# Performance work log

Measured on AMD Instinct MI355X. Metric: run time of the kernel, lower is better.

The kernel has to match this reference:

```python
import jax, jax.numpy as jnp
import numpy as np

B, D_IN, R, D_P, K, D_C, ITERS = 4096, 2048, 7, 128, 25, 16, 3


def _ln(x, g, b, eps=1e-5):
    m = jnp.mean(x, axis=-1, keepdims=True)
    v = jnp.var(x, axis=-1, keepdims=True)
    return (x - m) * jax.lax.rsqrt(v + eps) * g + b


def _squash(x):
    eps = 1e-6
    ns = jnp.sum(x * x, axis=-1, keepdims=True)
    scale = ns / jnp.maximum(1.0 + ns, eps)
    return scale * x / (jnp.sqrt(ns) + eps)


def setup_inputs() -> dict:
    key = jax.random.key(0)
    ks = jax.random.split(key, 8)
    f = lambda k, shp, s=0.02: (jax.random.normal(k, shp) * s).astype(jnp.float32)
    return {
        "z": jax.random.normal(ks[0], (B, D_IN), jnp.float32),
        "W_prim": f(ks[1], (D_IN, R * D_P)),
        "b_prim": jnp.zeros((R * D_P,), jnp.float32),
        "ln_a_g": jnp.ones((D_IN,), jnp.float32),
        "ln_a_b": jnp.zeros((D_IN,), jnp.float32),
        "W_act": f(ks[2], (D_IN, R)),
        "b_act": jnp.zeros((R,), jnp.float32),
        "w_caps": (np.sqrt(K / (D_P * R)).astype(np.float32)
                   * jax.random.normal(ks[3], (R, D_P, K, D_C))).astype(jnp.float32),
        "ln_c_g": jnp.ones((D_C,), jnp.float32),
        "ln_c_b": jnp.zeros((D_C,), jnp.float32),
        "beta_u": f(ks[4], (K,), 1.0),
        "ln_h_g": jnp.ones((R * D_C,), jnp.float32),
        "ln_h_b": jnp.zeros((R * D_C,), jnp.float32),
        "W_h1": f(ks[5], (R * D_C, 4 * R * D_C)),
        "b_h1": jnp.zeros((4 * R * D_C,), jnp.float32),
        "W_h2": f(ks[6], (4 * R * D_C, 1)),
        "b_h2": jnp.zeros((1,), jnp.float32),
    }


def reference(z, W_prim, b_prim, ln_a_g, ln_a_b, W_act, b_act, w_caps,
              ln_c_g, ln_c_b, beta_u, ln_h_g, ln_h_b, W_h1, b_h1, W_h2, b_h2):
    # primary capsules: [B, R, D_P] poses + [B, R] activations
    pose = _squash((z @ W_prim + b_prim).reshape(B, R, D_P))
    act = jnp.clip(jax.nn.sigmoid(_ln(z, ln_a_g, ln_a_b) @ W_act + b_act), 0.0, 1.0)

    # votes: [B, R, K, D_C]
    u = jnp.einsum('brd,rdkh->brkh', pose, w_caps)
    scale = 1.0 / np.sqrt(D_C).astype(np.float32)

    # iterative routing (EM/softmax-agreement style)
    q = jnp.full((B, R, K), 1.0 / K, dtype=z.dtype)
    class_pose = None
    for _ in range(ITERS):
        wts = q * act[:, :, None]                               # [B,R,K]
        class_pose = _ln(jnp.einsum('brk,brkh->bkh', wts, u), ln_c_g, ln_c_b)
        agree = jnp.einsum('bkh,brkh->brk', class_pose, u) * scale
        q = jax.nn.softmax(agree, axis=-1)

    class_act = jax.nn.sigmoid(beta_u[None, :] + jnp.einsum('brk,br->bk', q, act))
    route_class_emb = q[..., None] * u                          # [B,R,K,D_C]

    # concat per-route interaction vectors -> [B, K, R*D_C]
    class_embed = jnp.transpose(route_class_emb, (0, 2, 1, 3)).reshape(B, K, R * D_C)
    h = jax.nn.gelu(_ln(class_embed, ln_h_g, ln_h_b) @ W_h1 + b_h1, approximate=False)
    logits = (h @ W_h2 + b_h2)[..., 0]                          # [B, K]

    return (logits, class_embed, class_pose, class_act, q, pose, act, route_class_emb)
```

## Files before the change

kernel.cpp:

```cpp
#include <hip/hip_runtime.h>
#include <cstddef>

#define BB 4096
#define DIN 2048
#define RR 7
#define DP 128
#define KK 25
#define DC 16
#define NITERS 3
#define RKH (RR*KK*DC)
#define RK  (RR*KK)
#define KH  (KK*DC)
#define HD  (RR*DC)
#define H4  (4*HD)
#define HEAD_TILES (BB*KK/128)

typedef __attribute__((ext_vector_type(8))) short bf16x8;
typedef __attribute__((ext_vector_type(4))) float f32x4;

__device__ __forceinline__ unsigned pk_bf16(float a, float b) {
    union { float f; unsigned u; } xa, xb;
    xa.f = a; xb.f = b;
    unsigned ua = (xa.u + 0x7FFFu + ((xa.u >> 16) & 1u)) >> 16;
    unsigned ub = (xb.u + 0x7FFFu + ((xb.u >> 16) & 1u)) >> 16;
    return (ua & 0xFFFFu) | (ub << 16);
}

__device__ __forceinline__ float gelu_fast(float x) {
    float u = x * __builtin_fmaf(x * x, 0.07135655f, 1.5957691f);
    u = fmaxf(u, -30.0f);
    float e = __expf(-u);
    return x * __builtin_amdgcn_rcpf(1.0f + e);
}

__global__ __launch_bounds__(256) void transpose_cvt_kernel(
    const float* __restrict__ src, unsigned short* __restrict__ dst, int RS, int CS)
{
    __shared__ float T[64][65];
    int r0 = blockIdx.x * 64, c0 = blockIdx.y * 64;
    size_t bo = (size_t)blockIdx.z * RS * CS;
    src += bo; dst += bo;
    int t = threadIdx.x;
    for (int s = t; s < 64 * 16; s += 256) {
        int row = s >> 4, c4 = s & 15;
        int gr = r0 + row, gc = c0 + c4 * 4;
        float4 v = make_float4(0.f, 0.f, 0.f, 0.f);
        if (gr < RS && gc < CS) v = *(const float4*)(src + (size_t)gr * CS + gc);
        T[row][c4 * 4 + 0] = v.x; T[row][c4 * 4 + 1] = v.y;
        T[row][c4 * 4 + 2] = v.z; T[row][c4 * 4 + 3] = v.w;
    }
    __syncthreads();
    for (int s = t; s < 64 * 16; s += 256) {
        int col = s >> 4, r4 = s & 15;
        int gc = c0 + col, gr = r0 + r4 * 4;
        if (gc < CS && gr + 3 < RS) {
            unsigned lo = pk_bf16(T[r4 * 4 + 0][col], T[r4 * 4 + 1][col]);
            unsigned hi = pk_bf16(T[r4 * 4 + 2][col], T[r4 * 4 + 3][col]);
            *(uint2*)(dst + (size_t)gc * RS + gr) = make_uint2(lo, hi);
        }
    }
}

__global__ __launch_bounds__(256) void w1_frag_kernel(
    const float* __restrict__ W1, unsigned short* __restrict__ W1F)
{
    int d = blockIdx.x * 256 + threadIdx.x;
    int e2 = d & 3;
    int lane = (d >> 2) & 63;
    int fid = d >> 8;
    int j = fid & 3, ks = (fid >> 2) & 3, nc = fid >> 4;
    int col = nc * 64 + j * 16 + (lane & 15);
    int k = ks * 32 + (lane >> 4) * 8 + e2 * 2;
    float a = (k < HD)     ? W1[(size_t)k * H4 + col]       : 0.f;
    float b = (k + 1 < HD) ? W1[(size_t)(k + 1) * H4 + col] : 0.f;
    ((unsigned*)W1F)[d] = pk_bf16(a, b);
}

__global__ __launch_bounds__(256) void wpf_kernel(
    const float* __restrict__ Wp, unsigned short* __restrict__ wpf)
{
    int tid = blockIdx.x * 256 + threadIdx.x;
    int lane = tid & 63;
    int CH = tid >> 6;
    int c = CH & 63, gcol = CH >> 6;
    int n = gcol * 16 + (lane & 15);
    int k0 = c * 32 + (lane >> 4) * 8;
    unsigned d0, d1, d2, d3;
    {
        float a0 = Wp[(size_t)(k0 + 0) * (RR * DP) + n];
        float a1 = Wp[(size_t)(k0 + 1) * (RR * DP) + n];
        float a2 = Wp[(size_t)(k0 + 2) * (RR * DP) + n];
        float a3 = Wp[(size_t)(k0 + 3) * (RR * DP) + n];
        float a4 = Wp[(size_t)(k0 + 4) * (RR * DP) + n];
        float a5 = Wp[(size_t)(k0 + 5) * (RR * DP) + n];
        float a6 = Wp[(size_t)(k0 + 6) * (RR * DP) + n];
        float a7 = Wp[(size_t)(k0 + 7) * (RR * DP) + n];
        d0 = pk_bf16(a0, a1); d1 = pk_bf16(a2, a3);
        d2 = pk_bf16(a4, a5); d3 = pk_bf16(a6, a7);
    }
    *(uint4*)(wpf + (size_t)tid * 8) = make_uint4(d0, d1, d2, d3);
}

__global__ __launch_bounds__(256) void act_kernel(
    const float* __restrict__ z, const float* __restrict__ g, const float* __restrict__ bb,
    const float* __restrict__ Wa, const float* __restrict__ ba,
    float* __restrict__ act_out, unsigned short* __restrict__ zf_out)
{
    int b = blockIdx.x;
    int t = threadIdx.x;
    __shared__ float zs[DIN];
    __shared__ float ws1[4], ws2[4];
    __shared__ float wr[4][RR];
    const float* zr = z + (size_t)b * DIN;
    float s = 0.f, s2 = 0.f;
    for (int i = t; i < DIN; i += 256) {
        float v = zr[i]; zs[i] = v; s += v; s2 += v * v;
    }
    for (int off = 32; off; off >>= 1) { s += __shfl_down(s, off); s2 += __shfl_down(s2, off); }
    int w = t >> 6, lane = t & 63;
    if (lane == 0) { ws1[w] = s; ws2[w] = s2; }
    __syncthreads();
    if (zf_out) {
        int c = t >> 2, o = t & 3;
        const float* zp = zs + c * 32 + o * 8;
        unsigned d0 = pk_bf16(zp[0], zp[1]);
        unsigned d1 = pk_bf16(zp[2], zp[3]);
        unsigned d2 = pk_bf16(zp[4], zp[5]);
        unsigned d3 = pk_bf16(zp[6], zp[7]);
        size_t off2 = (((size_t)(b >> 4) * 64 + c) * 64 + (size_t)(o * 16 + (b & 15))) * 8;
        *(uint4*)(zf_out + off2) = make_uint4(d0, d1, d2, d3);
    }
    s  = ws1[0] + ws1[1] + ws1[2] + ws1[3];
    s2 = ws2[0] + ws2[1] + ws2[2] + ws2[3];
    float mean = s * (1.0f / DIN);
    float var  = s2 * (1.0f / DIN) - mean * mean;
    float rstd = rsqrtf(var + 1e-5f);
    float acc[RR];
#pragma unroll
    for (int r = 0; r < RR; ++r) acc[r] = 0.f;
    for (int i = t; i < DIN; i += 256) {
        float y = (zs[i] - mean) * rstd * g[i] + bb[i];
#pragma unroll
        for (int r = 0; r < RR; ++r) acc[r] += y * Wa[i * RR + r];
    }
    for (int off = 32; off; off >>= 1) {
#pragma unroll
        for (int r = 0; r < RR; ++r) acc[r] += __shfl_down(acc[r], off);
    }
    if (lane == 0) {
#pragma unroll
        for (int r = 0; r < RR; ++r) wr[w][r] = acc[r];
    }
    __syncthreads();
    if (t < RR) {
        float v = wr[0][t] + wr[1][t] + wr[2][t] + wr[3][t] + ba[t];
        float sg = 1.0f / (1.0f + expf(-v));
        sg = fminf(fmaxf(sg, 0.0f), 1.0f);
        act_out[(size_t)b * RR + t] = sg;
    }
}

#define POSE_STAGE(KS, BUF) do {                                                            \
    _Pragma("unroll")                                                                       \
    for (int q = 0; q < 4; ++q) {                                                           \
        int ch = w * 4 + q;                                                                 \
        int gi = ch >> 2, cc = ch & 3;                                                      \
        __builtin_amdgcn_global_load_lds(                                                   \
            (const __attribute__((address_space(1))) unsigned int*)(const void*)            \
                (zf + (((size_t)(zbase + gi) * 64) + (KS) * 4 + cc) * 512 + l * 8),         \
            (__attribute__((address_space(3))) unsigned int*)(void*)                        \
                (&As[BUF][ch * 512 + l * 8]), 16, 0, 0);                                    \
        __builtin_amdgcn_global_load_lds(                                                   \
            (const __attribute__((address_space(1))) unsigned int*)(const void*)            \
                (wpf + (((size_t)(wbase + gi) * 64) + (KS) * 4 + cc) * 512 + l * 8),        \
            (__attribute__((address_space(3))) unsigned int*)(void*)                        \
                (&Bs[BUF][ch * 512 + l * 8]), 16, 0, 0);                                    \
    }                                                                                       \
} while (0)

__global__ __launch_bounds__(512) void pose_mfma2(
    const unsigned short* __restrict__ zf, const unsigned short* __restrict__ wpf,
    const float* __restrict__ bp, float* __restrict__ pose_out)
{
    __shared__ __align__(16) unsigned short As[2][32 * 512];
    __shared__ __align__(16) unsigned short Bs[2][32 * 512];
    __shared__ float sq[2][128];
    int m0 = blockIdx.x * 128, r = blockIdx.y;
    int t = threadIdx.x, w = t >> 6, l = t & 63;
    int wr = w >> 1, wc = w & 1;
    int lrow = l & 15, koff = l >> 4;
    int zbase = m0 >> 4;
    int wbase = r * 8;

    f32x4 acc[2][4];
#pragma unroll
    for (int i = 0; i < 2; ++i)
#pragma unroll
        for (int j = 0; j < 4; ++j) acc[i][j] = 0.0f;

    POSE_STAGE(0, 0);
    __syncthreads();
    for (int ks = 0; ks < 16; ++ks) {
        int cur = ks & 1;
        if (ks < 15) POSE_STAGE(ks + 1, cur ^ 1);
#pragma unroll
        for (int c = 0; c < 4; ++c) {
            bf16x8 a[2], b[4];
#pragma unroll
            for (int i = 0; i < 2; ++i)
                a[i] = *(const bf16x8*)(&As[cur][((wr * 2 + i) * 4 + c) * 512 + l * 8]);
#pragma unroll
            for (int j = 0; j < 4; ++j)
                b[j] = *(const bf16x8*)(&Bs[cur][((wc * 4 + j) * 4 + c) * 512 + l * 8]);
#pragma unroll
            for (int i = 0; i < 2; ++i)
#pragma unroll
                for (int j = 0; j < 4; ++j)
                    acc[i][j] = __builtin_amdgcn_mfma_f32_16x16x32_bf16(a[i], b[j], acc[i][j], 0, 0, 0);
        }
        __syncthreads();
    }
    float bpv[4];
#pragma unroll
    for (int j = 0; j < 4; ++j) bpv[j] = bp[r * DP + wc * 64 + j * 16 + lrow];
    float ns_[2][4];
#pragma unroll
    for (int i = 0; i < 2; ++i)
#pragma unroll
        for (int reg = 0; reg < 4; ++reg) {
            float ss = 0.f;
#pragma unroll
            for (int j = 0; j < 4; ++j) {
                float x = acc[i][j][reg] + bpv[j];
                acc[i][j][reg] = x;
                ss += x * x;
            }
            ss += __shfl_xor(ss, 1); ss += __shfl_xor(ss, 2);
            ss += __shfl_xor(ss, 4); ss += __shfl_xor(ss, 8);
            ns_[i][reg] = ss;
        }
    if (lrow == 0) {
#pragma unroll
        for (int i = 0; i < 2; ++i)
#pragma unroll
            for (int reg = 0; reg < 4; ++reg)
                sq[wc][wr * 32 + i * 16 + koff * 4 + reg] = ns_[i][reg];
    }
    __syncthreads();
#pragma unroll
    for (int i = 0; i < 2; ++i)
#pragma unroll
        for (int reg = 0; reg < 4; ++reg) {
            int rl = wr * 32 + i * 16 + koff * 4 + reg;
            float ns = sq[0][rl] + sq[1][rl];
            float factor = (ns / fmaxf(1.0f + ns, 1e-6f)) / (sqrtf(ns) + 1e-6f);
            size_t rowbase = ((size_t)(m0 + rl) * RR + r) * DP;
#pragma unroll
            for (int j = 0; j < 4; ++j)
                pose_out[rowbase + wc * 64 + j * 16 + lrow] = acc[i][j][reg] * factor;
        }
}

__global__ __launch_bounds__(256) void pose_mfma(
    const float* __restrict__ z, const unsigned short* __restrict__ WpT,
    const float* __restrict__ bp, float* __restrict__ pose_out)
{
    __shared__ __align__(16) unsigned short As[128 * 40];
    __shared__ __align__(16) unsigned short Bs[128 * 40];
    __shared__ float sq[2][128];
    int m0 = blockIdx.x * 128, r = blockIdx.y, t = threadIdx.x;
    int n0 = r * DP;
    int w = t >> 6, l = t & 63;
    int lrow = l & 15, koff = l >> 4;
    int rbase = (w >> 1) * 64, cbase = (w & 1) * 64;
    f32x4 acc[4][4];
#pragma unroll
    for (int i = 0; i < 4; ++i)
#pragma unroll
        for (int j = 0; j < 4; ++j) acc[i][j] = 0.0f;
    for (int kt = 0; kt < DIN; kt += 32) {
#pragma unroll
        for (int q = 0; q < 4; ++q) {
            int s = t + 256 * q;
            int row = s >> 3, k4 = s & 7;
            float4 v = *(const float4*)(z + (size_t)(m0 + row) * DIN + kt + k4 * 4);
            *(uint2*)(As + row * 40 + k4 * 4) = make_uint2(pk_bf16(v.x, v.y), pk_bf16(v.z, v.w));
        }
#pragma unroll
        for (int q = 0; q < 2; ++q) {
            int s = t + 256 * q;
            int col = s >> 2, k8 = s & 3;
            uint4 v = *(const uint4*)(WpT + (size_t)(n0 + col) * DIN + kt + k8 * 8);
            *(uint4*)(Bs + col * 40 + k8 * 8) = v;
        }
        __syncthreads();
        bf16x8 a[4], b[4];
#pragma unroll
        for (int i = 0; i < 4; ++i)
            a[i] = *(const bf16x8*)(As + (rbase + i * 16 + lrow) * 40 + koff * 8);
#pragma unroll
        for (int j = 0; j < 4; ++j)
            b[j] = *(const bf16x8*)(Bs + (cbase + j * 16 + lrow) * 40 + koff * 8);
#pragma unroll
        for (int i = 0; i < 4; ++i)
#pragma unroll
            for (int j = 0; j < 4; ++j)
                acc[i][j] = __builtin_amdgcn_mfma_f32_16x16x32_bf16(a[i], b[j], acc[i][j], 0, 0, 0);
        __syncthreads();
    }
    float bpv[4];
#pragma unroll
    for (int j = 0; j < 4; ++j) bpv[j] = bp[n0 + cbase + j * 16 + lrow];
    float ns_[4][4];
#pragma unroll
    for (int i = 0; i < 4; ++i)
#pragma unroll
        for (int reg = 0; reg < 4; ++reg) {
            float ss = 0.f;
#pragma unroll
            for (int j = 0; j < 4; ++j) {
                float x = acc[i][j][reg] + bpv[j];
                acc[i][j][reg] = x;
                ss += x * x;
            }
            ss += __shfl_xor(ss, 1); ss += __shfl_xor(ss, 2);
            ss += __shfl_xor(ss, 4); ss += __shfl_xor(ss, 8);
            ns_[i][reg] = ss;
        }
    if (lrow == 0) {
#pragma unroll
        for (int i = 0; i < 4; ++i)
#pragma unroll
            for (int reg = 0; reg < 4; ++reg)
                sq[w & 1][rbase + i * 16 + koff * 4 + reg] = ns_[i][reg];
    }
    __syncthreads();
#pragma unroll
    for (int i = 0; i < 4; ++i)
#pragma unroll
        for (int reg = 0; reg < 4; ++reg) {
            int rl = rbase + i * 16 + koff * 4 + reg;
            float ns = sq[0][rl] + sq[1][rl];
            float factor = (ns / fmaxf(1.0f + ns, 1e-6f)) / (sqrtf(ns) + 1e-6f);
            size_t rowbase = ((size_t)(m0 + rl) * RR + r) * DP;
#pragma unroll
            for (int j = 0; j < 4; ++j)
                pose_out[rowbase + cbase + j * 16 + lrow] = acc[i][j][reg] * factor;
        }
}

__global__ __launch_bounds__(256) void votes_mfma(
    const float* __restrict__ pose, const unsigned short* __restrict__ wcT,
    float* __restrict__ u_out)
{
    __shared__ __align__(16) unsigned short As[128 * 152];
    __shared__ __align__(16) unsigned short Bs[80 * 152];
    int m0 = blockIdx.x * 128, r = blockIdx.y, n0 = blockIdx.z * 80;
    int t = threadIdx.x;
    int w = t >> 6, l = t & 63;
    int lrow = l & 15, koff = l >> 4;
    int rbase = w * 32;
#pragma unroll
    for (int q = 0; q < 16; ++q) {
        int s = t + 256 * q;
        int row = s >> 5, k4 = s & 31;
        float4 v = *(const float4*)(pose + ((size_t)(m0 + row) * RR + r) * DP + k4 * 4);
        *(uint2*)(As + row * 152 + k4 * 4) = make_uint2(pk_bf16(v.x, v.y), pk_bf16(v.z, v.w));
    }
    const unsigned short* wr_ = wcT + (size_t)r * KH * DP;
#pragma unroll
    for (int q = 0; q < 5; ++q) {
        int s = t + 256 * q;
        int col = s >> 4, k8 = s & 15;
        uint4 v = *(const uint4*)(wr_ + (size_t)(n0 + col) * DP + k8 * 8);
        *(uint4*)(Bs + col * 152 + k8 * 8) = v;
    }
    __syncthreads();
    f32x4 acc[2][5];
#pragma unroll
    for (int i = 0; i < 2; ++i)
#pragma unroll
        for (int j = 0; j < 5; ++j) acc[i][j] = 0.0f;
#pragma unroll
    for (int ks = 0; ks < 4; ++ks) {
        bf16x8 a[2], b[5];
#pragma unroll
        for (int i = 0; i < 2; ++i)
            a[i] = *(const bf16x8*)(As + (rbase + i * 16 + lrow) * 152 + ks * 32 + koff * 8);
#pragma unroll
        for (int j = 0; j < 5; ++j)
            b[j] = *(const bf16x8*)(Bs + (j * 16 + lrow) * 152 + ks * 32 + koff * 8);
#pragma unroll
        for (int i = 0; i < 2; ++i)
#pragma unroll
            for (int j = 0; j < 5; ++j)
                acc[i][j] = __builtin_amdgcn_mfma_f32_16x16x32_bf16(a[i], b[j], acc[i][j], 0, 0, 0);
    }
#pragma unroll
    for (int i = 0; i < 2; ++i)
#pragma unroll
        for (int reg = 0; reg < 4; ++reg) {
            int row = m0 + rbase + i * 16 + koff * 4 + reg;
            size_t base = ((size_t)row * RR + r) * KH + n0;
#pragma unroll
            for (int j = 0; j < 5; ++j)
                u_out[base + j * 16 + lrow] = acc[i][j][reg];
        }
}

__global__ __launch_bounds__(64) void routing_kernel(
    const float* __restrict__ u_in, const float* __restrict__ act_in,
    const float* __restrict__ lncg, const float* __restrict__ lncb,
    const float* __restrict__ beta_u,
    float* __restrict__ q_out, float* __restrict__ cp_out,
    float* __restrict__ ca_out, float* __restrict__ rce_out,
    float* __restrict__ ce_out)
{
    __shared__ __align__(16) float U[RKH];
    __shared__ float Q[RK];
    __shared__ float CP[KH];
    __shared__ float AG[RK];
    __shared__ float A7[RR];
    int b = blockIdx.x, t = threadIdx.x;
    const float4* u4 = (const float4*)(u_in + (size_t)b * RKH);
    float4* U4 = (float4*)U;
    for (int p = t; p < RKH / 4; p += 64) U4[p] = u4[p];
    if (t < RR) A7[t] = act_in[(size_t)b * RR + t];
    for (int p = t; p < RK; p += 64) Q[p] = 1.0f / KK;
    __syncthreads();
    for (int it = 0; it < NITERS; ++it) {
        for (int p = t; p < KH; p += 64) {
            int k = p / DC;
            float s = 0.f;
#pragma unroll
            for (int r = 0; r < RR; ++r) s += Q[r * KK + k] * A7[r] * U[r * KH + p];
            CP[p] = s;
        }
        __syncthreads();
        if (t < KK) {
            float m = 0.f;
#pragma unroll
            for (int h = 0; h < DC; ++h) m += CP[t * DC + h];
            m *= (1.0f / DC);
            float v = 0.f;
#pragma unroll
            for (int h = 0; h < DC; ++h) { float d = CP[t * DC + h] - m; v += d * d; }
            v *= (1.0f / DC);
            float rstd = rsqrtf(v + 1e-5f);
#pragma unroll
            for (int h = 0; h < DC; ++h)
                CP[t * DC + h] = (CP[t * DC + h] - m) * rstd * lncg[h] + lncb[h];
        }
        __syncthreads();
        for (int p = t; p < RK; p += 64) {
            int r = p / KK, k = p % KK;
            float s = 0.f;
#pragma unroll
            for (int h = 0; h < DC; ++h) s += CP[k * DC + h] * U[r * KH + k * DC + h];
            AG[p] = s * 0.25f;
        }
        __syncthreads();
        if (t < RR) {
            float mx = -1e30f;
            for (int k = 0; k < KK; ++k) mx = fmaxf(mx, AG[t * KK + k]);
            float e[KK], sum = 0.f;
            for (int k = 0; k < KK; ++k) { e[k] = expf(AG[t * KK + k] - mx); sum += e[k]; }
            float inv = 1.0f / sum;
            for (int k = 0; k < KK; ++k) Q[t * KK + k] = e[k] * inv;
        }
        __syncthreads();
    }
    if (t < KK) {
        float s = 0.f;
#pragma unroll
        for (int r = 0; r < RR; ++r) s += Q[r * KK + t] * A7[r];
        ca_out[(size_t)b * KK + t] = 1.0f / (1.0f + expf(-(beta_u[t] + s)));
    }
    for (int p = t; p < RK; p += 64) q_out[(size_t)b * RK + p] = Q[p];
    for (int p = t; p < KH; p += 64) cp_out[(size_t)b * KH + p] = CP[p];
    float4* rce4 = (float4*)(rce_out + (size_t)b * RKH);
    float4* ce4  = (float4*)ce_out;
    for (int p4 = t; p4 < RKH / 4; p4 += 64) {
        int base = p4 * 4;
        int r  = base / KH;
        int k  = (base % KH) / DC;
        int h0 = base % DC;
        float qv = Q[r * KK + k];
        float4 uv = U4[p4];
        float4 rv = make_float4(qv * uv.x, qv * uv.y, qv * uv.z, qv * uv.w);
        rce4[p4] = rv;
        size_t ci = ((size_t)b * RKH + (size_t)k * HD + (size_t)r * DC + h0) >> 2;
        ce4[ci] = rv;
    }
}

__global__ __launch_bounds__(512) void head_mfma(
    const float* __restrict__ ce, const float* __restrict__ g, const float* __restrict__ bb,
    const unsigned short* __restrict__ W1F, const float* __restrict__ b1,
    const float* __restrict__ W2, const float* __restrict__ b2,
    float* __restrict__ logits)
{
    __shared__ __align__(16) unsigned short As[128 * 128];
    __shared__ __align__(16) unsigned short Bs[448 * 128];
    __shared__ float LB1[H4];
    __shared__ float LW2[H4];
    int t = threadIdx.x;
    int w = t >> 6, l = t & 63;
    int lrow = l & 15, koff = l >> 4;

#pragma unroll
    for (int q = 0; q < 14; ++q) {
        int chunk = w * 14 + q;
        __builtin_amdgcn_global_load_lds(
            (const __attribute__((address_space(1))) unsigned int*)(const void*)(W1F + (size_t)chunk * 512 + l * 8),
            (__attribute__((address_space(3))) unsigned int*)(void*)(Bs + chunk * 512),
            16, 0, 0);
    }
    if (t >= 256) {
        for (int s = t - 256; s < H4; s += 256) { LB1[s] = b1[s]; LW2[s] = W2[s]; }
    }
    float b2v = b2[0];

    int row = t >> 1, half = t & 1;
    int lr = row & 15, rt = row >> 4;

    float4 v[14];
    int tile = blockIdx.x;
    if (t < 256 && tile < HEAD_TILES) {
        const float* rp = ce + (size_t)(tile * 128 + row) * HD + half * 56;
#pragma unroll
        for (int m = 0; m < 14; ++m) v[m] = *(const float4*)(rp + m * 4);
    }

    bool first = true;
    for (; tile < HEAD_TILES; tile += 256) {
        if (!first) __syncthreads();
        first = false;

        if (t < 256) {
            float s1 = 0.f, s2 = 0.f;
#pragma unroll
            for (int m = 0; m < 14; ++m) {
                s1 += v[m].x + v[m].y + v[m].z + v[m].w;
                s2 += v[m].x * v[m].x + v[m].y * v[m].y + v[m].z * v[m].z + v[m].w * v[m].w;
            }
            s1 += __shfl_xor(s1, 1); s2 += __shfl_xor(s2, 1);
            float mean = s1 * (1.0f / HD);
            float var  = s2 * (1.0f / HD) - mean * mean;
            float rstd = rsqrtf(var + 1e-5f);
#pragma unroll
            for (int j = 0; j < 7; ++j) {
                float4 gl0 = *(const float4*)(g  + half * 56 + j * 8);
                float4 gl1 = *(const float4*)(g  + half * 56 + j * 8 + 4);
                float4 bl0 = *(const float4*)(bb + half * 56 + j * 8);
                float4 bl1 = *(const float4*)(bb + half * 56 + j * 8 + 4);
                float4 x0 = v[j * 2], x1 = v[j * 2 + 1];
                float y0 = (x0.x - mean) * rstd * gl0.x + bl0.x;
                float y1 = (x0.y - mean) * rstd * gl0.y + bl0.y;
                float y2 = (x0.z - mean) * rstd * gl0.z + bl0.z;
                float y3 = (x0.w - mean) * rstd * gl0.w + bl0.w;
                float y4 = (x1.x - mean) * rstd * gl1.x + bl1.x;
                float y5 = (x1.y - mean) * rstd * gl1.y + bl1.y;
                float y6 = (x1.z - mean) * rstd * gl1.z + bl1.z;
                float y7 = (x1.w - mean) * rstd * gl1.w + bl1.w;
                int k8 = half * 7 + j;
                int ks = k8 >> 2, ko = k8 & 3;
                unsigned* dst = (unsigned*)(As + (size_t)((rt * 4 + ks) * 64 + ko * 16 + lr) * 8);
                dst[0] = pk_bf16(y0, y1); dst[1] = pk_bf16(y2, y3);
                dst[2] = pk_bf16(y4, y5); dst[3] = pk_bf16(y6, y7);
            }
            if (half) {
                uint4 z4 = make_uint4(0, 0, 0, 0);
                *(uint4*)(As + (size_t)((rt * 4 + 3) * 64 + 2 * 16 + lr) * 8) = z4;
                *(uint4*)(As + (size_t)((rt * 4 + 3) * 64 + 3 * 16 + lr) * 8) = z4;
            }
        }
        __syncthreads();

        bf16x8 af[4];
#pragma unroll
        for (int ks = 0; ks < 4; ++ks)
            af[ks] = *(const bf16x8*)(As + (size_t)((w * 4 + ks) * 64 + l) * 8);

        if (t < 256 && tile + 256 < HEAD_TILES) {
            const float* rp = ce + (size_t)((tile + 256) * 128 + row) * HD + half * 56;
#pragma unroll
            for (int m = 0; m < 14; ++m) v[m] = *(const float4*)(rp + m * 4);
        }

        float logitAcc[4];
#pragma unroll
        for (int reg = 0; reg < 4; ++reg) logitAcc[reg] = 0.f;

        for (int nc = 0; nc < 7; ++nc) {
            float b1v[4], w2v[4];
#pragma unroll
            for (int j = 0; j < 4; ++j) {
                b1v[j] = LB1[nc * 64 + j * 16 + lrow];
                w2v[j] = LW2[nc * 64 + j * 16 + lrow];
            }
            f32x4 acc[4];
#pragma unroll
            for (int j = 0; j < 4; ++j) acc[j] = 0.0f;
#pragma unroll
            for (int ks = 0; ks < 4; ++ks) {
                bf16x8 bfr[4];
#pragma unroll
                for (int j = 0; j < 4; ++j)
                    bfr[j] = *(const bf16x8*)(Bs + (size_t)(((nc * 4 + ks) * 4 + j) * 64 + l) * 8);
#pragma unroll
                for (int j = 0; j < 4; ++j)
                    acc[j] = __builtin_amdgcn_mfma_f32_16x16x32_bf16(af[ks], bfr[j], acc[j], 0, 0, 0);
            }
#pragma unroll
            for (int reg = 0; reg < 4; ++reg) {
                float sum = 0.f;
#pragma unroll
                for (int j = 0; j < 4; ++j) {
                    float x = acc[j][reg] + b1v[j];
                    sum += gelu_fast(x) * w2v[j];
                }
                logitAcc[reg] += sum;
            }
        }
#pragma unroll
        for (int reg = 0; reg < 4; ++reg) {
            float vv = logitAcc[reg];
            vv += __shfl_xor(vv, 1); vv += __shfl_xor(vv, 2);
            vv += __shfl_xor(vv, 4); vv += __shfl_xor(vv, 8);
            if (lrow == 0)
                logits[(size_t)tile * 128 + w * 16 + koff * 4 + reg] = vv + b2v;
        }
    }
}

__global__ __launch_bounds__(256) void pose_kernel(
    const float* __restrict__ z, const float* __restrict__ Wp, const float* __restrict__ bp,
    float* __restrict__ pose_out)
{
    __shared__ __align__(16) float As[64 * 36];
    __shared__ __align__(16) float Bs[32 * 128];
    int m0 = blockIdx.x * 64;
    int r  = blockIdx.y;
    int n0 = r * DP;
    int t  = threadIdx.x;
    int rg = t >> 5;
    int cg = t & 31;
    float acc[8][4] = {};
    for (int kt = 0; kt < DIN; kt += 32) {
#pragma unroll
        for (int q = 0; q < 2; ++q) {
            int s = t * 2 + q;
            int row = s >> 3, k4 = s & 7;
            float4 v = *(const float4*)(z + (size_t)(m0 + row) * DIN + kt + k4 * 4);
            *(float4*)(As + row * 36 + k4 * 4) = v;
        }
#pragma unroll
        for (int q = 0; q < 4; ++q) {
            int s = t + 256 * q;
            int row = s >> 5, c4 = s & 31;
            float4 v = *(const float4*)(Wp + (size_t)(kt + row) * (RR * DP) + n0 + c4 * 4);
            *(float4*)(Bs + row * 128 + c4 * 4) = v;
        }
        __syncthreads();
#pragma unroll
        for (int kk = 0; kk < 32; ++kk) {
            float4 bv = *(const float4*)(Bs + kk * 128 + cg * 4);
#pragma unroll
            for (int j = 0; j < 8; ++j) {
                float a = As[(rg * 8 + j) * 36 + kk];
                acc[j][0] += a * bv.x; acc[j][1] += a * bv.y;
                acc[j][2] += a * bv.z; acc[j][3] += a * bv.w;
            }
        }
        __syncthreads();
    }
    float bi0 = bp[n0 + cg * 4], bi1 = bp[n0 + cg * 4 + 1];
    float bi2 = bp[n0 + cg * 4 + 2], bi3 = bp[n0 + cg * 4 + 3];
#pragma unroll
    for (int j = 0; j < 8; ++j) {
        float x0 = acc[j][0] + bi0, x1 = acc[j][1] + bi1;
        float x2 = acc[j][2] + bi2, x3 = acc[j][3] + bi3;
        float ns = x0 * x0 + x1 * x1 + x2 * x2 + x3 * x3;
        for (int off = 1; off < 32; off <<= 1) ns += __shfl_xor(ns, off);
        float factor = (ns / fmaxf(1.0f + ns, 1e-6f)) / (sqrtf(ns) + 1e-6f);
        int row = m0 + rg * 8 + j;
        float4 o = make_float4(x0 * factor, x1 * factor, x2 * factor, x3 * factor);
        *(float4*)(pose_out + ((size_t)row * RR + r) * DP + cg * 4) = o;
    }
}

__global__ __launch_bounds__(256) void votes_kernel(
    const float* __restrict__ pose, const float* __restrict__ wc,
    float* __restrict__ u_out)
{
    __shared__ float As[64 * 129];
    __shared__ __align__(16) float Bs[64 * 80];
    int m0 = blockIdx.x * 64;
    int r  = blockIdx.y;
    int n0 = blockIdx.z * 80;
    int t  = threadIdx.x;
    const size_t wbase = (size_t)r * DP * KH;
#pragma unroll
    for (int q = 0; q < 8; ++q) {
        int s = t + 256 * q;
        int row = s >> 5, d4 = s & 31;
        float4 v = *(const float4*)(pose + ((size_t)(m0 + row) * RR + r) * DP + d4 * 4);
        As[row * 129 + d4 * 4 + 0] = v.x;
        As[row * 129 + d4 * 4 + 1] = v.y;
        As[row * 129 + d4 * 4 + 2] = v.z;
        As[row * 129 + d4 * 4 + 3] = v.w;
    }
    int m4 = t >> 4, n5 = t & 15;
    float acc[4][5];
#pragma unroll
    for (int i = 0; i < 4; ++i)
#pragma unroll
        for (int j = 0; j < 5; ++j) acc[i][j] = 0.f;
    for (int kt = 0; kt < DP; kt += 64) {
        __syncthreads();
#pragma unroll
        for (int q = 0; q < 5; ++q) {
            int s = t + 256 * q;
            int d = s / 20, c4 = s % 20;
            float4 v = *(const float4*)(wc + wbase + (size_t)(kt + d) * KH + n0 + c4 * 4);
            *(float4*)(Bs + d * 80 + c4 * 4) = v;
        }
        __syncthreads();
#pragma unroll 4
        for (int dd = 0; dd < 64; ++dd) {
            int d = kt + dd;
            float b_[5];
#pragma unroll
            for (int j = 0; j < 5; ++j) b_[j] = Bs[dd * 80 + n5 * 5 + j];
#pragma unroll
            for (int i = 0; i < 4; ++i) {
                float a = As[(m4 * 4 + i) * 129 + d];
#pragma unroll
                for (int j = 0; j < 5; ++j) acc[i][j] += a * b_[j];
            }
        }
    }
#pragma unroll
    for (int i = 0; i < 4; ++i) {
        int row = m0 + m4 * 4 + i;
        size_t base = ((size_t)row * RR + r) * KH + n0 + n5 * 5;
#pragma unroll
        for (int j = 0; j < 5; ++j) u_out[base + j] = acc[i][j];
    }
}

__global__ __launch_bounds__(256) void head_kernel(
    const float* __restrict__ ce, const float* __restrict__ g, const float* __restrict__ bb,
    const float* __restrict__ W1, const float* __restrict__ b1,
    const float* __restrict__ W2, const float* __restrict__ b2,
    float* __restrict__ logits)
{
    __shared__ __align__(16) float Y[64 * HD];
    __shared__ float Wc[HD * 64];
    __shared__ float Lg[64];
    int row0 = blockIdx.x * 64;
    int t = threadIdx.x;
    for (int s = t; s < 64 * HD; s += 256) Y[s] = ce[(size_t)row0 * HD + s];
    __syncthreads();
    if (t < 64) {
        float m = 0.f;
        for (int i = 0; i < HD; ++i) m += Y[t * HD + i];
        m *= (1.0f / HD);
        float v = 0.f;
        for (int i = 0; i < HD; ++i) { float d = Y[t * HD + i] - m; v += d * d; }
        v *= (1.0f / HD);
        float rstd = rsqrtf(v + 1e-5f);
        for (int i = 0; i < HD; ++i) Y[t * HD + i] = (Y[t * HD + i] - m) * rstd * g[i] + bb[i];
    }
    int rg = t >> 4;
    int cg = t & 15;
    float accRow[4] = {0.f, 0.f, 0.f, 0.f};
    for (int c0 = 0; c0 < H4; c0 += 64) {
        __syncthreads();
        for (int s = t; s < HD * 64; s += 256) {
            int i = s >> 6, c = s & 63;
            Wc[i * 64 + c] = W1[(size_t)i * H4 + c0 + c];
        }
        __syncthreads();
        float b1v[4], w2v[4];
#pragma unroll
        for (int c = 0; c < 4; ++c) { b1v[c] = b1[c0 + cg * 4 + c]; w2v[c] = W2[c0 + cg * 4 + c]; }
        float s_[4][4];
#pragma unroll
        for (int rr = 0; rr < 4; ++rr)
#pragma unroll
            for (int c = 0; c < 4; ++c) s_[rr][c] = b1v[c];
        for (int i4 = 0; i4 < HD / 4; ++i4) {
            float4 y4[4];
#pragma unroll
            for (int rr = 0; rr < 4; ++rr)
                y4[rr] = *(const float4*)(Y + (rg * 4 + rr) * HD + i4 * 4);
#pragma unroll
            for (int is = 0; is < 4; ++is) {
                float w_[4];
#pragma unroll
                for (int c = 0; c < 4; ++c) w_[c] = Wc[(i4 * 4 + is) * 64 + cg * 4 + c];
#pragma unroll
                for (int rr = 0; rr < 4; ++rr) {
                    float yv = (is == 0) ? y4[rr].x : (is == 1) ? y4[rr].y : (is == 2) ? y4[rr].z : y4[rr].w;
#pragma unroll
                    for (int c = 0; c < 4; ++c) s_[rr][c] += yv * w_[c];
                }
            }
        }
#pragma unroll
        for (int rr = 0; rr < 4; ++rr) {
#pragma unroll
            for (int c = 0; c < 4; ++c) {
                float x = s_[rr][c];
                float ge = 0.5f * x * (1.0f + erff(x * 0.70710678118654752440f));
                accRow[rr] += ge * w2v[c];
            }
        }
    }
#pragma unroll
    for (int rr = 0; rr < 4; ++rr) {
        float v = accRow[rr];
        v += __shfl_xor(v, 1); v += __shfl_xor(v, 2);
        v += __shfl_xor(v, 4); v += __shfl_xor(v, 8);
        if (cg == 0) Lg[rg * 4 + rr] = v;
    }
    __syncthreads();
    if (t < 64) logits[row0 + t] = Lg[t] + b2[0];
}

extern "C" void kernel_launch(void* const* d_in, const int* in_sizes, int n_in,
                              void* d_out, int out_size, void* d_ws, size_t ws_size,
                              hipStream_t stream) {
    const float* z    = (const float*)d_in[0];
    const float* Wp   = (const float*)d_in[1];
    const float* bp   = (const float*)d_in[2];
    const float* lnag = (const float*)d_in[3];
    const float* lnab = (const float*)d_in[4];
    const float* Wa   = (const float*)d_in[5];
    const float* ba   = (const float*)d_in[6];
    const float* wc   = (const float*)d_in[7];
    const float* lncg = (const float*)d_in[8];
    const float* lncb = (const float*)d_in[9];
    const float* beta = (const float*)d_in[10];
    const float* lnhg = (const float*)d_in[11];
    const float* lnhb = (const float*)d_in[12];
    const float* W1   = (const float*)d_in[13];
    const float* b1   = (const float*)d_in[14];
    const float* W2   = (const float*)d_in[15];
    const float* b2   = (const float*)d_in[16];

    float* out = (float*)d_out;
    float* o_logits = out;
    float* o_ce   = o_logits + (size_t)BB * KK;
    float* o_cp   = o_ce   + (size_t)BB * KK * HD;
    float* o_ca   = o_cp   + (size_t)BB * KK * DC;
    float* o_q    = o_ca   + (size_t)BB * KK;
    float* o_pose = o_q    + (size_t)BB * RK;
    float* o_act  = o_pose + (size_t)BB * RR * DP;
    float* o_rce  = o_act  + (size_t)BB * RR;

    const size_t W1F_ELE = (size_t)H4 * 128;
    const size_t WCT_ELE = (size_t)RR * KH * DP;
    const size_t ZF_ELE  = (size_t)BB * DIN;
    const size_t WPF_ELE = (size_t)(RR * DP) * DIN;
    const size_t WPT_ELE = WPF_ELE;
    unsigned short* W1F = (unsigned short*)d_ws;
    unsigned short* wcT = W1F + W1F_ELE;
    unsigned short* zf  = wcT + WCT_ELE;
    unsigned short* wpf = zf + ZF_ELE;
    unsigned short* WpT = zf;

    const size_t WS_NEW = (W1F_ELE + WCT_ELE + ZF_ELE + WPF_ELE) * sizeof(unsigned short);
    const size_t WS_MID = (W1F_ELE + WCT_ELE + WPT_ELE) * sizeof(unsigned short);

    if (ws_size >= WS_NEW) {
        hipLaunchKernelGGL(act_kernel, dim3(BB), dim3(256), 0, stream,
                           z, lnag, lnab, Wa, ba, o_act, zf);
        hipLaunchKernelGGL(wpf_kernel, dim3(896), dim3(256), 0, stream, Wp, wpf);
        hipLaunchKernelGGL(w1_frag_kernel, dim3(112), dim3(256), 0, stream, W1, W1F);
        hipLaunchKernelGGL(transpose_cvt_kernel, dim3(2, 7, RR), dim3(256), 0, stream,
                           wc, wcT, DP, KH);
        hipLaunchKernelGGL(pose_mfma2, dim3(BB / 128, RR), dim3(512), 0, stream,
                           zf, wpf, bp, o_pose);
        hipLaunchKernelGGL(votes_mfma, dim3(BB / 128, RR, 5), dim3(256), 0, stream,
                           o_pose, wcT, o_rce);
        hipLaunchKernelGGL(routing_kernel, dim3(BB), dim3(64), 0, stream,
                           o_rce, o_act, lncg, lncb, beta, o_q, o_cp, o_ca, o_rce, o_ce);
        hipLaunchKernelGGL(head_mfma, dim3(256), dim3(512), 0, stream,
                           o_ce, lnhg, lnhb, W1F, b1, W2, b2, o_logits);
    } else if (ws_size >= WS_MID) {
        hipLaunchKernelGGL(act_kernel, dim3(BB), dim3(256), 0, stream,
                           z, lnag, lnab, Wa, ba, o_act, (unsigned short*)nullptr);
        hipLaunchKernelGGL(transpose_cvt_kernel, dim3(DIN / 64, (RR * DP) / 64, 1), dim3(256), 0, stream,
                           Wp, WpT, DIN, RR * DP);
        hipLaunchKernelGGL(w1_frag_kernel, dim3(112), dim3(256), 0, stream, W1, W1F);
        hipLaunchKernelGGL(transpose_cvt_kernel, dim3(2, 7, RR), dim3(256), 0, stream,
                           wc, wcT, DP, KH);
        hipLaunchKernelGGL(pose_mfma, dim3(BB / 128, RR), dim3(256), 0, stream,
                           z, WpT, bp, o_pose);
        hipLaunchKernelGGL(votes_mfma, dim3(BB / 128, RR, 5), dim3(256), 0, stream,
                           o_pose, wcT, o_rce);
        hipLaunchKernelGGL(routing_kernel, dim3(BB), dim3(64), 0, stream,
                           o_rce, o_act, lncg, lncb, beta, o_q, o_cp, o_ca, o_rce, o_ce);
        hipLaunchKernelGGL(head_mfma, dim3(256), dim3(512), 0, stream,
                           o_ce, lnhg, lnhb, W1F, b1, W2, b2, o_logits);
    } else {
        hipLaunchKernelGGL(act_kernel, dim3(BB), dim3(256), 0, stream,
                           z, lnag, lnab, Wa, ba, o_act, (unsigned short*)nullptr);
        hipLaunchKernelGGL(pose_kernel, dim3(BB / 64, RR), dim3(256), 0, stream,
                           z, Wp, bp, o_pose);
        hipLaunchKernelGGL(votes_kernel, dim3(BB / 64, RR, 5), dim3(256), 0, stream,
                           o_pose, wc, o_rce);
        hipLaunchKernelGGL(routing_kernel, dim3(BB), dim3(64), 0, stream,
                           o_rce, o_act, lncg, lncb, beta, o_q, o_cp, o_ca, o_rce, o_ce);
        hipLaunchKernelGGL(head_kernel, dim3(BB * KK / 64), dim3(256), 0, stream,
                           o_ce, lnhg, lnhb, W1, b1, W2, b2, o_logits);
    }
}
```

Before: 326.8 us.

## Fuse votes GEMM into pose kernel using LDS-resident bf16 pose tile

Replaces the separate votes_mfma launch with an epilogue in the pose kernel. After squashing, each block writes its pose tile as bf16 MFMA fragments into LDS, streams a fragment-packed w_caps slice (made by a new wcf_kernel) into LDS, and computes the votes directly. This avoids re-reading pose from global memory and one kernel launch. In exchange it uses about 132KB of LDS per block, which limits occupancy, and the votes loop runs on only 7x32 blocks.

Result: faster. 315.1 us (-3.6%).

```diff
diff --git a/kernel.cpp b/kernel.cpp
--- a/kernel.cpp
+++ b/kernel.cpp
@@ -24,6 +24,11 @@
     unsigned ua = (xa.u + 0x7FFFu + ((xa.u >> 16) & 1u)) >> 16;
     unsigned ub = (xb.u + 0x7FFFu + ((xb.u >> 16) & 1u)) >> 16;
     return (ua & 0xFFFFu) | (ub << 16);
+}
+
+__device__ __forceinline__ unsigned short bf16_1(float a) {
+    union { float f; unsigned u; } xa; xa.f = a;
+    return (unsigned short)((xa.u + 0x7FFFu + ((xa.u >> 16) & 1u)) >> 16);
 }
 
 __device__ __forceinline__ float gelu_fast(float x) {
@@ -101,6 +106,34 @@
     *(uint4*)(wpf + (size_t)tid * 8) = make_uint4(d0, d1, d2, d3);
 }
 
+__global__ __launch_bounds__(256) void wcf_kernel(
+    const float* __restrict__ wc, unsigned short* __restrict__ wcf)
+{
+    __shared__ float Sw[128][17];
+    int r = blockIdx.x, nt = blockIdx.y;
+    int t = threadIdx.x;
+    {
+        int d = t >> 1, half = t & 1;
+        const float* sp = wc + ((size_t)r * DP + d) * KH + nt * 16 + half * 8;
+        float4 v0 = *(const float4*)(sp);
+        float4 v1 = *(const float4*)(sp + 4);
+        Sw[d][half * 8 + 0] = v0.x; Sw[d][half * 8 + 1] = v0.y;
+        Sw[d][half * 8 + 2] = v0.z; Sw[d][half * 8 + 3] = v0.w;
+        Sw[d][half * 8 + 4] = v1.x; Sw[d][half * 8 + 5] = v1.y;
+        Sw[d][half * 8 + 6] = v1.z; Sw[d][half * 8 + 7] = v1.w;
+    }
+    __syncthreads();
+    int l = t >> 2, e2 = t & 3;
+    int n = l & 15;
+    unsigned* outp = (unsigned*)wcf;
+#pragma unroll
+    for (int c = 0; c < 4; ++c) {
+        int d = c * 32 + (l >> 4) * 8 + e2 * 2;
+        unsigned v = pk_bf16(Sw[d][n], Sw[d + 1][n]);
+        outp[(size_t)((r * 100 + nt * 4 + c)) * 256 + t] = v;
+    }
+}
+
 __global__ __launch_bounds__(256) void act_kernel(
     const float* __restrict__ z, const float* __restrict__ g, const float* __restrict__ bb,
     const float* __restrict__ Wa, const float* __restrict__ ba,
@@ -160,7 +193,7 @@
     }
 }
 
-#define POSE_STAGE(KS, BUF) do {                                                            \
+#define PV_STAGE(KS, AD, BD) do {                                                           \
     _Pragma("unroll")                                                                       \
     for (int q = 0; q < 4; ++q) {                                                           \
         int ch = w * 4 + q;                                                                 \
@@ -169,25 +202,50 @@
             (const __attribute__((address_space(1))) unsigned int*)(const void*)            \
                 (zf + (((size_t)(zbase + gi) * 64) + (KS) * 4 + cc) * 512 + l * 8),         \
             (__attribute__((address_space(3))) unsigned int*)(void*)                        \
-                (&As[BUF][ch * 512 + l * 8]), 16, 0, 0);                                    \
+                ((AD) + ch * 512 + l * 8), 16, 0, 0);                                       \
         __builtin_amdgcn_global_load_lds(                                                   \
             (const __attribute__((address_space(1))) unsigned int*)(const void*)            \
                 (wpf + (((size_t)(wbase + gi) * 64) + (KS) * 4 + cc) * 512 + l * 8),        \
             (__attribute__((address_space(3))) unsigned int*)(void*)                        \
-                (&Bs[BUF][ch * 512 + l * 8]), 16, 0, 0);                                    \
+                ((BD) + ch * 512 + l * 8), 16, 0, 0);                                       \
     }                                                                                       \
 } while (0)
 
-__global__ __launch_bounds__(512) void pose_mfma2(
+#define PV_COMPUTE(AD, BD) do {                                                             \
+    _Pragma("unroll")                                                                       \
+    for (int c = 0; c < 4; ++c) {                                                           \
+        bf16x8 a[2], b[4];                                                                  \
+        _Pragma("unroll")                                                                   \
+        for (int i = 0; i < 2; ++i)                                                         \
+            a[i] = *(const bf16x8*)((AD) + ((wrI * 2 + i) * 4 + c) * 512 + l * 8);          \
+        _Pragma("unroll")                                                                   \
+        for (int j = 0; j < 4; ++j)                                                         \
+            b[j] = *(const bf16x8*)((BD) + ((wcI * 4 + j) * 4 + c) * 512 + l * 8);          \
+        _Pragma("unroll")                                                                   \
+        for (int i = 0; i < 2; ++i)                                                         \
+            _Pragma("unroll")                                                               \
+            for (int j = 0; j < 4; ++j)                                                     \
+                acc[i][j] = __builtin_amdgcn_mfma_f32_16x16x32_bf16(a[i], b[j], acc[i][j], 0, 0, 0); \
+    }                                                                                       \
+} while (0)
+
+__global__ __launch_bounds__(512) void pose_votes_mfma(
     const unsigned short* __restrict__ zf, const unsigned short* __restrict__ wpf,
-    const float* __restrict__ bp, float* __restrict__ pose_out)
-{
-    __shared__ __align__(16) unsigned short As[2][32 * 512];
-    __shared__ __align__(16) unsigned short Bs[2][32 * 512];
+    const unsigned short* __restrict__ wcf, const float* __restrict__ bp,
+    float* __restrict__ pose_out, float* __restrict__ u_out)
+{
+    __shared__ __align__(16) char pool[135168];
     __shared__ float sq[2][128];
+    unsigned short* A0 = (unsigned short*)pool;
+    unsigned short* A1 = (unsigned short*)(pool + 32768);
+    unsigned short* B0 = (unsigned short*)(pool + 65536);
+    unsigned short* B1 = (unsigned short*)(pool + 98304);
+    unsigned short* AT = (unsigned short*)pool;
+    unsigned short* BV = (unsigned short*)(pool + 32768);
+
     int m0 = blockIdx.x * 128, r = blockIdx.y;
     int t = threadIdx.x, w = t >> 6, l = t & 63;
-    int wr = w >> 1, wc = w & 1;
+    int wrI = w >> 1, wcI = w & 1;
     int lrow = l & 15, koff = l >> 4;
     int zbase = m0 >> 4;
     int wbase = r * 8;
@@ -198,31 +256,32 @@
 #pragma unroll
         for (int j = 0; j < 4; ++j) acc[i][j] = 0.0f;
 
-    POSE_STAGE(0, 0);
-    __syncthreads();
-    for (int ks = 0; ks < 16; ++ks) {
-        int cur = ks & 1;
-        if (ks < 15) POSE_STAGE(ks + 1, cur ^ 1);
-#pragma unroll
-        for (int c = 0; c < 4; ++c) {
-            bf16x8 a[2], b[4];
-#pragma unroll
-            for (int i = 0; i < 2; ++i)
-                a[i] = *(const bf16x8*)(&As[cur][((wr * 2 + i) * 4 + c) * 512 + l * 8]);
-#pragma unroll
-            for (int j = 0; j < 4; ++j)
-                b[j] = *(const bf16x8*)(&Bs[cur][((wc * 4 + j) * 4 + c) * 512 + l * 8]);
-#pragma unroll
-            for (int i = 0; i < 2; ++i)
-#pragma unroll
-                for (int j = 0; j < 4; ++j)
-                    acc[i][j] = __builtin_amdgcn_mfma_f32_16x16x32_bf16(a[i], b[j], acc[i][j], 0, 0, 0);
-        }
-        __syncthreads();
-    }
+    PV_STAGE(0, A0, B0);
+    __syncthreads();
+#pragma unroll 1
+    for (int ks = 0; ks < 16; ks += 2) {
+        if (ks + 1 < 16) PV_STAGE(ks + 1, A1, B1);
+        PV_COMPUTE(A0, B0);
+        __syncthreads();
+        if (ks + 2 < 16) PV_STAGE(ks + 2, A0, B0);
+        PV_COMPUTE(A1, B1);
+        __syncthreads();
+    }
+
+    const unsigned short* wrp = wcf + (size_t)r * 100 * 512;
+#pragma unroll
+    for (int q = 0; q < 13; ++q) {
+        int chunk = w + q * 8;
+        if (chunk < 100)
+            __builtin_amdgcn_global_load_lds(
+                (const __attribute__((address_space(1))) unsigned int*)(const void*)(wrp + (size_t)chunk * 512 + l * 8),
+                (__attribute__((address_space(3))) unsigned int*)(void*)(BV + chunk * 512),
+                16, 0, 0);
+    }
+
     float bpv[4];
 #pragma unroll
-    for (int j = 0; j < 4; ++j) bpv[j] = bp[r * DP + wc * 64 + j * 16 + lrow];
+    for (int j = 0; j < 4; ++j) bpv[j] = bp[r * DP + wcI * 64 + j * 16 + lrow];
     float ns_[2][4];
 #pragma unroll
     for (int i = 0; i < 2; ++i)
@@ -244,21 +303,50 @@
         for (int i = 0; i < 2; ++i)
 #pragma unroll
             for (int reg = 0; reg < 4; ++reg)
-                sq[wc][wr * 32 + i * 16 + koff * 4 + reg] = ns_[i][reg];
-    }
-    __syncthreads();
+                sq[wcI][wrI * 32 + i * 16 + koff * 4 + reg] = ns_[i][reg];
+    }
+    __syncthreads();
+
 #pragma unroll
     for (int i = 0; i < 2; ++i)
 #pragma unroll
         for (int reg = 0; reg < 4; ++reg) {
-            int rl = wr * 32 + i * 16 + koff * 4 + reg;
+            int rl = wrI * 32 + i * 16 + koff * 4 + reg;
             float ns = sq[0][rl] + sq[1][rl];
             float factor = (ns / fmaxf(1.0f + ns, 1e-6f)) / (sqrtf(ns) + 1e-6f);
             size_t rowbase = ((size_t)(m0 + rl) * RR + r) * DP;
-#pragma unroll
-            for (int j = 0; j < 4; ++j)
-                pose_out[rowbase + wc * 64 + j * 16 + lrow] = acc[i][j][reg] * factor;
-        }
+            int g8 = rl >> 4, r15 = rl & 15;
+#pragma unroll
+            for (int j = 0; j < 4; ++j) {
+                float v = acc[i][j][reg] * factor;
+                int col = wcI * 64 + j * 16 + lrow;
+                pose_out[rowbase + col] = v;
+                int cseg = col >> 5;
+                int l2 = r15 + 16 * ((col >> 3) & 3);
+                AT[(size_t)((g8 * 4 + cseg) * 64 + l2) * 8 + (col & 7)] = bf16_1(v);
+            }
+        }
+    __syncthreads();
+
+    bf16x8 af2[4];
+#pragma unroll
+    for (int c = 0; c < 4; ++c)
+        af2[c] = *(const bf16x8*)(AT + (size_t)((w * 4 + c) * 64 + l) * 8);
+    int crow = (l >> 4) * 4;
+#pragma unroll 1
+    for (int nt = 0; nt < 25; ++nt) {
+        f32x4 a2 = 0.0f;
+#pragma unroll
+        for (int c = 0; c < 4; ++c) {
+            bf16x8 bfr = *(const bf16x8*)(BV + (size_t)((nt * 4 + c) * 64 + l) * 8);
+            a2 = __builtin_amdgcn_mfma_f32_16x16x32_bf16(af2[c], bfr, a2, 0, 0, 0);
+        }
+#pragma unroll
+        for (int reg = 0; reg < 4; ++reg) {
+            int row = m0 + w * 16 + crow + reg;
+            u_out[((size_t)row * RR + r) * KH + nt * 16 + (l & 15)] = a2[reg];
+        }
+    }
 }
 
 __global__ __launch_bounds__(256) void pose_mfma(
@@ -862,30 +950,27 @@
     float* o_rce  = o_act  + (size_t)BB * RR;
 
     const size_t W1F_ELE = (size_t)H4 * 128;
-    const size_t WCT_ELE = (size_t)RR * KH * DP;
+    const size_t WCF_ELE = (size_t)RR * 100 * 512;
     const size_t ZF_ELE  = (size_t)BB * DIN;
     const size_t WPF_ELE = (size_t)(RR * DP) * DIN;
-    const size_t WPT_ELE = WPF_ELE;
     unsigned short* W1F = (unsigned short*)d_ws;
-    unsigned short* wcT = W1F + W1F_ELE;
-    unsigned short* zf  = wcT + WCT_ELE;
+    unsigned short* wcf = W1F + W1F_ELE;
+    unsigned short* zf  = wcf + WCF_ELE;
     unsigned short* wpf = zf + ZF_ELE;
+    unsigned short* wcT = wcf;
     unsigned short* WpT = zf;
 
-    const size_t WS_NEW = (W1F_ELE + WCT_ELE + ZF_ELE + WPF_ELE) * sizeof(unsigned short);
-    const size_t WS_MID = (W1F_ELE + WCT_ELE + WPT_ELE) * sizeof(unsigned short);
+    const size_t WS_NEW = (W1F_ELE + WCF_ELE + ZF_ELE + WPF_ELE) * sizeof(unsigned short);
+    const size_t WS_MID = (W1F_ELE + WCF_ELE + WPF_ELE) * sizeof(unsigned short);
 
     if (ws_size >= WS_NEW) {
         hipLaunchKernelGGL(act_kernel, dim3(BB), dim3(256), 0, stream,
                            z, lnag, lnab, Wa, ba, o_act, zf);
         hipLaunchKernelGGL(wpf_kernel, dim3(896), dim3(256), 0, stream, Wp, wpf);
         hipLaunchKernelGGL(w1_frag_kernel, dim3(112), dim3(256), 0, stream, W1, W1F);
-        hipLaunchKernelGGL(transpose_cvt_kernel, dim3(2, 7, RR), dim3(256), 0, stream,
-                           wc, wcT, DP, KH);
-        hipLaunchKernelGGL(pose_mfma2, dim3(BB / 128, RR), dim3(512), 0, stream,
-                           zf, wpf, bp, o_pose);
-        hipLaunchKernelGGL(votes_mfma, dim3(BB / 128, RR, 5), dim3(256), 0, stream,
-                           o_pose, wcT, o_rce);
+        hipLaunchKernelGGL(wcf_kernel, dim3(RR, 25), dim3(256), 0, stream, wc, wcf);
+        hipLaunchKernelGGL(pose_votes_mfma, dim3(BB / 128, RR), dim3(512), 0, stream,
+                           zf, wpf, wcf, bp, o_pose, o_rce);
         hipLaunchKernelGGL(routing_kernel, dim3(BB), dim3(64), 0, stream,
                            o_rce, o_act, lncg, lncb, beta, o_q, o_cp, o_ca, o_rce, o_ce);
         hipLaunchKernelGGL(head_mfma, dim3(256), dim3(512), 0, stream,
```
